# Performance work log

Hardware: AMD Instinct MI355X
Metric: run time of the kernel (lower is better)

## Reference

```python
import jax, jax.numpy as jnp
import numpy as np

B, N, C, H, W = 4, 5, 64, 100, 252  # N agents per sample (uniform record_len)


def setup_inputs() -> dict:
    key = jax.random.key(0)
    k1, k2, k3 = jax.random.split(key, 3)
    x = jax.random.normal(k1, (B * N, C, H, W), dtype=jnp.float32)
    rm = jax.random.normal(k2, (B * N, 2, H, W), dtype=jnp.float32)
    record_len = jnp.full((B,), N, dtype=jnp.int32)
    # normalized 2x3 affines (identity + small perturbation), shape (B, L, L, 2, 3)
    eye = jnp.broadcast_to(jnp.array([[1.0, 0.0, 0.0], [0.0, 1.0, 0.0]], jnp.float32), (B, N, N, 2, 3))
    pairwise_t_matrix = eye + 0.05 * jax.random.normal(k3, (B, N, N, 2, 3), dtype=jnp.float32)
    return {"x": x, "rm": rm, "record_len": record_len, "pairwise_t_matrix": pairwise_t_matrix}


def _warp_affine(feats, theta):
    # feats: (N, C, H, W), theta: (N, 2, 3). torch affine_grid + grid_sample,
    # bilinear, zeros padding, align_corners=False.
    xs = (2.0 * jnp.arange(W, dtype=jnp.float32) + 1.0) / W - 1.0
    ys = (2.0 * jnp.arange(H, dtype=jnp.float32) + 1.0) / H - 1.0
    gy, gx = jnp.meshgrid(ys, xs, indexing="ij")           # (H, W)
    base = jnp.stack([gx, gy, jnp.ones_like(gx)], axis=-1)  # (H, W, 3)
    coords = jnp.einsum("nij,hwj->nhwi", theta, base)       # (N, H, W, 2) normalized
    ix = ((coords[..., 0] + 1.0) * W - 1.0) * 0.5            # input pixel coords
    iy = ((coords[..., 1] + 1.0) * H - 1.0) * 0.5
    x0 = jnp.floor(ix); y0 = jnp.floor(iy)
    x1 = x0 + 1.0;      y1 = y0 + 1.0
    wx1 = ix - x0; wx0 = 1.0 - wx1
    wy1 = iy - y0; wy0 = 1.0 - wy1

    def gather(xi, yi):
        valid = (xi >= 0) & (xi <= W - 1) & (yi >= 0) & (yi <= H - 1)
        xc = jnp.clip(xi, 0, W - 1).astype(jnp.int32)
        yc = jnp.clip(yi, 0, H - 1).astype(jnp.int32)
        v = jax.vmap(lambda f, yy, xx: f[:, yy, xx])(feats, yc, xc)  # (N, C, H, W)
        return v * valid[:, None, :, :].astype(feats.dtype)

    out = (gather(x0, y0) * (wx0 * wy0)[:, None]
         + gather(x1, y0) * (wx1 * wy0)[:, None]
         + gather(x0, y1) * (wx0 * wy1)[:, None]
         + gather(x1, y1) * (wx1 * wy1)[:, None])
    return out  # (N, C, H, W)


def reference(x, rm, record_len, pairwise_t_matrix):
    # Where2commFusion, single-scale, MAX agg, communication disabled.
    # regroup: uniform record_len -> reshape (B, N, C, H, W)
    xr = x.reshape(B, N, C, H, W)
    theta = pairwise_t_matrix[:, 0, :, :, :]  # t_matrix[0, :N] per batch: (B, N, 2, 3)
    warped = jax.vmap(_warp_affine)(xr, theta)  # (B, N, C, H, W)
    x_fuse = jnp.max(warped, axis=1)            # (B, C, H, W)
    communication_rates = jnp.zeros((), dtype=jnp.float32)
    return (x_fuse, communication_rates)
```

## Files before the change

### kernel.cpp

```cpp
#include <hip/hip_runtime.h>
#include <math.h>

#define BB 4
#define NN 5
#define CC_DIM 64
#define HH 100
#define WW 252
#define HW (HH * WW)
#define CPT 8
#define NCHUNK (CC_DIM / CPT)

__global__ __launch_bounds__(256) void where2comm_fuse_kernel(
    const float* __restrict__ x,
    const float* __restrict__ ptm,
    float* __restrict__ out)
{
    const int idx = blockIdx.x * blockDim.x + threadIdx.x;
    const int total = BB * NCHUNK * HH * WW;
    if (idx >= total) {
        return;
    }

    int w = idx % WW;
    int t = idx / WW;
    int h = t % HH;
    t /= HH;
    int cc = t % NCHUNK;
    int b = t / NCHUNK;

    const float gx = (2.0f * (float)w + 1.0f) / (float)WW - 1.0f;
    const float gy = (2.0f * (float)h + 1.0f) / (float)HH - 1.0f;

    const float* th_b = ptm + (size_t)b * (NN * NN * 6);

    const float* pbase[NN];
    float g00[NN], g01[NN], g10[NN], g11[NN];

#pragma unroll
    for (int n = 0; n < NN; ++n) {
        const float t00 = th_b[n * 6 + 0];
        const float t01 = th_b[n * 6 + 1];
        const float t02 = th_b[n * 6 + 2];
        const float t10 = th_b[n * 6 + 3];
        const float t11 = th_b[n * 6 + 4];
        const float t12 = th_b[n * 6 + 5];

        const float cx = t00 * gx + t01 * gy + t02;
        const float cy = t10 * gx + t11 * gy + t12;

        const float ix = ((cx + 1.0f) * (float)WW - 1.0f) * 0.5f;
        const float iy = ((cy + 1.0f) * (float)HH - 1.0f) * 0.5f;

        const float x0f = floorf(ix);
        const float y0f = floorf(iy);
        const float x1f = x0f + 1.0f;
        const float y1f = y0f + 1.0f;

        const float wx1 = ix - x0f;
        const float wx0 = 1.0f - wx1;
        const float wy1 = iy - y0f;
        const float wy0 = 1.0f - wy1;

        const float mx0 = (x0f >= 0.0f && x0f <= (float)(WW - 1)) ? 1.0f : 0.0f;
        const float mx1 = (x1f >= 0.0f && x1f <= (float)(WW - 1)) ? 1.0f : 0.0f;
        const float my0 = (y0f >= 0.0f && y0f <= (float)(HH - 1)) ? 1.0f : 0.0f;
        const float my1 = (y1f >= 0.0f && y1f <= (float)(HH - 1)) ? 1.0f : 0.0f;

        const float e00 = wx0 * wy0 * mx0 * my0;
        const float e10 = wx1 * wy0 * mx1 * my0;
        const float e01 = wx0 * wy1 * mx0 * my1;
        const float e11 = wx1 * wy1 * mx1 * my1;

        const int xi0 = (int)fminf(fmaxf(x0f, 0.0f), (float)(WW - 1));
        const int xi1 = (int)fminf(fmaxf(x1f, 0.0f), (float)(WW - 1));
        const int yi0 = (int)fminf(fmaxf(y0f, 0.0f), (float)(HH - 1));
        const int yi1 = (int)fminf(fmaxf(y1f, 0.0f), (float)(HH - 1));

        const int cl = (int)fminf(fmaxf(x0f, 0.0f), (float)(WW - 2));
        const int rl = (int)fminf(fmaxf(y0f, 0.0f), (float)(HH - 2));

        const float sx0 = (float)(xi0 - cl);
        const float sx1 = (float)(xi1 - cl);
        const float sy0 = (float)(yi0 - rl);
        const float sy1 = (float)(yi1 - rl);
        const float nx0 = 1.0f - sx0, nx1 = 1.0f - sx1;
        const float ny0 = 1.0f - sy0, ny1 = 1.0f - sy1;

        g00[n] = e00 * nx0 * ny0 + e10 * nx1 * ny0 + e01 * nx0 * ny1 + e11 * nx1 * ny1;
        g01[n] = e00 * sx0 * ny0 + e10 * sx1 * ny0 + e01 * sx0 * ny1 + e11 * sx1 * ny1;
        g10[n] = e00 * nx0 * sy0 + e10 * nx1 * sy0 + e01 * nx0 * sy1 + e11 * nx1 * sy1;
        g11[n] = e00 * sx0 * sy0 + e10 * sx1 * sy0 + e01 * sx0 * sy1 + e11 * sx1 * sy1;

        pbase[n] = x + ((size_t)(b * NN + n) * CC_DIM + cc * CPT) * HW + rl * WW + cl;
    }

    float acc[CPT];
#pragma unroll
    for (int c = 0; c < CPT; ++c) acc[c] = -INFINITY;

#pragma unroll
    for (int c = 0; c < CPT; ++c) {
        float lo[NN][2], hi[NN][2];
#pragma unroll
        for (int n = 0; n < NN; ++n) {
            const float* p = pbase[n] + (size_t)c * HW;
            __builtin_memcpy(&lo[n][0], p, 8);
            __builtin_memcpy(&hi[n][0], p + WW, 8);
        }
#pragma unroll
        for (int n = 0; n < NN; ++n) {
            float v = lo[n][0] * g00[n];
            v = fmaf(lo[n][1], g01[n], v);
            v = fmaf(hi[n][0], g10[n], v);
            v = fmaf(hi[n][1], g11[n], v);
            acc[c] = fmaxf(acc[c], v);
        }
    }

#pragma unroll
    for (int c = 0; c < CPT; ++c) {
        out[(((size_t)b * CC_DIM + cc * CPT + c) * HH + h) * WW + w] = acc[c];
    }

    if (idx == 0) {
        out[(size_t)BB * CC_DIM * HW] = 0.0f;
    }
}

extern "C" void kernel_launch(void* const* d_in, const int* in_sizes, int n_in,
                              void* d_out, int out_size, void* d_ws, size_t ws_size,
                              hipStream_t stream) {
    const float* x = (const float*)d_in[0];
    const float* ptm = (const float*)d_in[3];
    float* out = (float*)d_out;

    const int total = BB * NCHUNK * HH * WW;
    const int block = 256;
    const int grid = (total + block - 1) / block;
    where2comm_fuse_kernel<<<grid, block, 0, stream>>>(x, ptm, out);
}
```

Baseline: 59.29 us.

## Stage per-channel row tiles in LDS via async global-to-LDS loads for bilinear gather

```diff
diff --git a/kernel.cpp b/kernel.cpp
--- a/kernel.cpp
+++ b/kernel.cpp
@@ -7,122 +7,151 @@
 #define HH 100
 #define WW 252
 #define HW (HH * WW)
-#define CPT 8
-#define NCHUNK (CC_DIM / CPT)
+#define TH 25
+#define NT (HH / TH)
+#define PAD 12
+#define MAXR (TH + 2 * PAD + 1)
+#define PITCH 256
 
 __global__ __launch_bounds__(256) void where2comm_fuse_kernel(
     const float* __restrict__ x,
     const float* __restrict__ ptm,
     float* __restrict__ out)
 {
-    const int idx = blockIdx.x * blockDim.x + threadIdx.x;
-    const int total = BB * NCHUNK * HH * WW;
-    if (idx >= total) {
-        return;
-    }
+    __shared__ float smem[MAXR * PITCH];
 
-    int w = idx % WW;
-    int t = idx / WW;
-    int h = t % HH;
-    t /= HH;
-    int cc = t % NCHUNK;
-    int b = t / NCHUNK;
+    const int bi = blockIdx.x;
+    const int tile = bi % NT;
+    const int c = (bi / NT) % CC_DIM;
+    const int b = bi / (NT * CC_DIM);
+
+    const int h0 = tile * TH;
+    const int lo = (h0 - PAD > 0) ? (h0 - PAD) : 0;
+    const int hi = (h0 + TH + PAD < HH - 1) ? (h0 + TH + PAD) : (HH - 1);
+    const int nrows = hi - lo + 1;
+
+    const int tid = threadIdx.x;
+    const int lane = tid & 63;
+    const int wv = tid >> 6;
+    const int w = tid;
 
     const float gx = (2.0f * (float)w + 1.0f) / (float)WW - 1.0f;
-    const float gy = (2.0f * (float)h + 1.0f) / (float)HH - 1.0f;
+    const float gy0 = (2.0f * (float)h0 + 1.0f) / (float)HH - 1.0f;
 
     const float* th_b = ptm + (size_t)b * (NN * NN * 6);
 
-    const float* pbase[NN];
-    float g00[NN], g01[NN], g10[NN], g11[NN];
+    float acc[TH];
+#pragma unroll
+    for (int r = 0; r < TH; ++r) acc[r] = -INFINITY;
+
+    for (int n = 0; n < NN; ++n) {
+        const size_t plane_f = ((size_t)(b * NN + n) * CC_DIM + c) * HW;
+
+        for (int r = wv; r < nrows; r += 4) {
+            const float* src = x + plane_f + (size_t)(lo + r) * WW + lane * 4;
+            if (lane < 63) {
+                __builtin_amdgcn_global_load_lds(
+                    (const __attribute__((address_space(1))) void*)src,
+                    (__attribute__((address_space(3))) void*)(smem + r * PITCH),
+                    16, 0, 0);
+            }
+        }
+        asm volatile("s_waitcnt vmcnt(0)" ::: "memory");
+        __syncthreads();
+
+        if (w < WW) {
+            const float t00 = th_b[n * 6 + 0];
+            const float t01 = th_b[n * 6 + 1];
+            const float t02 = th_b[n * 6 + 2];
+            const float t10 = th_b[n * 6 + 3];
+            const float t11 = th_b[n * 6 + 4];
+            const float t12 = th_b[n * 6 + 5];
+
+            const float cx0 = fmaf(t00, gx, t02);
+            const float cy0 = fmaf(t10, gx, t12);
+            const float* plane = x + plane_f;
 
 #pragma unroll
-    for (int n = 0; n < NN; ++n) {
-        const float t00 = th_b[n * 6 + 0];
-        const float t01 = th_b[n * 6 + 1];
-        const float t02 = th_b[n * 6 + 2];
-        const float t10 = th_b[n * 6 + 3];
-        const float t11 = th_b[n * 6 + 4];
-        const float t12 = th_b[n * 6 + 5];
+            for (int r = 0; r < TH; ++r) {
+                const float gyr = fmaf((float)(2 * r), 0.01f, gy0);
+                const float cx = fmaf(t01, gyr, cx0);
+                const float cy = fmaf(t11, gyr, cy0);
+                const float ix = fmaf(cx, 126.0f, 125.5f);
+                const float iy = fmaf(cy, 50.0f, 49.5f);
 
-        const float cx = t00 * gx + t01 * gy + t02;
-        const float cy = t10 * gx + t11 * gy + t12;
+                const float x0f = floorf(ix);
+                const float y0f = floorf(iy);
+                const float x1f = x0f + 1.0f;
+                const float y1f = y0f + 1.0f;
 
-        const float ix = ((cx + 1.0f) * (float)WW - 1.0f) * 0.5f;
-        const float iy = ((cy + 1.0f) * (float)HH - 1.0f) * 0.5f;
+                const float wx1 = ix - x0f;
+                const float wx0 = 1.0f - wx1;
+                const float wy1 = iy - y0f;
+                const float wy0 = 1.0f - wy1;
 
-        const float x0f = floorf(ix);
-        const float y0f = floorf(iy);
-        const float x1f = x0f + 1.0f;
-        const float y1f = y0f + 1.0f;
+                const float mx0 = (x0f >= 0.0f && x0f <= (float)(WW - 1)) ? 1.0f : 0.0f;
+                const float mx1 = (x1f >= 0.0f && x1f <= (float)(WW - 1)) ? 1.0f : 0.0f;
+                const float my0 = (y0f >= 0.0f && y0f <= (float)(HH - 1)) ? 1.0f : 0.0f;
+                const float my1 = (y1f >= 0.0f && y1f <= (float)(HH - 1)) ? 1.0f : 0.0f;
 
-        const float wx1 = ix - x0f;
-        const float wx0 = 1.0f - wx1;
-        const float wy1 = iy - y0f;
-        const float wy0 = 1.0f - wy1;
+                const float e00 = wx0 * wy0 * mx0 * my0;
+                const float e10 = wx1 * wy0 * mx1 * my0;
+                const float e01 = wx0 * wy1 * mx0 * my1;
+                const float e11 = wx1 * wy1 * mx1 * my1;
 
-        const float mx0 = (x0f >= 0.0f && x0f <= (float)(WW - 1)) ? 1.0f : 0.0f;
-        const float mx1 = (x1f >= 0.0f && x1f <= (float)(WW - 1)) ? 1.0f : 0.0f;
-        const float my0 = (y0f >= 0.0f && y0f <= (float)(HH - 1)) ? 1.0f : 0.0f;
-        const float my1 = (y1f >= 0.0f && y1f <= (float)(HH - 1)) ? 1.0f : 0.0f;
+                const int xi0 = (int)fminf(fmaxf(x0f, 0.0f), (float)(WW - 1));
+                const int xi1 = (int)fminf(fmaxf(x1f, 0.0f), (float)(WW - 1));
+                const int yi0 = (int)fminf(fmaxf(y0f, 0.0f), (float)(HH - 1));
+                const int yi1 = (int)fminf(fmaxf(y1f, 0.0f), (float)(HH - 1));
 
-        const float e00 = wx0 * wy0 * mx0 * my0;
-        const float e10 = wx1 * wy0 * mx1 * my0;
-        const float e01 = wx0 * wy1 * mx0 * my1;
-        const float e11 = wx1 * wy1 * mx1 * my1;
+                const int cl = (int)fminf(fmaxf(x0f, 0.0f), (float)(WW - 2));
+                const int rl = (int)fminf(fmaxf(y0f, 0.0f), (float)(HH - 2));
 
-        const int xi0 = (int)fminf(fmaxf(x0f, 0.0f), (float)(WW - 1));
-        const int xi1 = (int)fminf(fmaxf(x1f, 0.0f), (float)(WW - 1));
-        const int yi0 = (int)fminf(fmaxf(y0f, 0.0f), (float)(HH - 1));
-        const int yi1 = (int)fminf(fmaxf(y1f, 0.0f), (float)(HH - 1));
+                const float sx0 = (float)(xi0 - cl);
+                const float sx1 = (float)(xi1 - cl);
+                const float sy0 = (float)(yi0 - rl);
+                const float sy1 = (float)(yi1 - rl);
+                const float nx0 = 1.0f - sx0, nx1 = 1.0f - sx1;
+                const float ny0 = 1.0f - sy0, ny1 = 1.0f - sy1;
 
-        const int cl = (int)fminf(fmaxf(x0f, 0.0f), (float)(WW - 2));
-        const int rl = (int)fminf(fmaxf(y0f, 0.0f), (float)(HH - 2));
+                const float g00 = e00 * nx0 * ny0 + e10 * nx1 * ny0 + e01 * nx0 * ny1 + e11 * nx1 * ny1;
+                const float g01 = e00 * sx0 * ny0 + e10 * sx1 * ny0 + e01 * sx0 * ny1 + e11 * sx1 * ny1;
+                const float g10 = e00 * nx0 * sy0 + e10 * nx1 * sy0 + e01 * nx0 * sy1 + e11 * nx1 * sy1;
+                const float g11 = e00 * sx0 * sy0 + e10 * sx1 * sy0 + e01 * sx0 * sy1 + e11 * sx1 * sy1;
 
-        const float sx0 = (float)(xi0 - cl);
-        const float sx1 = (float)(xi1 - cl);
-        const float sy0 = (float)(yi0 - rl);
-        const float sy1 = (float)(yi1 - rl);
-        const float nx0 = 1.0f - sx0, nx1 = 1.0f - sx1;
-        const float ny0 = 1.0f - sy0, ny1 = 1.0f - sy1;
+                float l00, l01, l10, l11;
+                if (rl >= lo && rl + 1 <= hi) {
+                    const float* sp = smem + (rl - lo) * PITCH + cl;
+                    l00 = sp[0];
+                    l01 = sp[1];
+                    l10 = sp[PITCH];
+                    l11 = sp[PITCH + 1];
+                } else {
+                    const float* gp = plane + (size_t)rl * WW + cl;
+                    l00 = gp[0];
+                    l01 = gp[1];
+                    l10 = gp[WW];
+                    l11 = gp[WW + 1];
+                }
 
-        g00[n] = e00 * nx0 * ny0 + e10 * nx1 * ny0 + e01 * nx0 * ny1 + e11 * nx1 * ny1;
-        g01[n] = e00 * sx0 * ny0 + e10 * sx1 * ny0 + e01 * sx0 * ny1 + e11 * sx1 * ny1;
-        g10[n] = e00 * nx0 * sy0 + e10 * nx1 * sy0 + e01 * nx0 * sy1 + e11 * nx1 * sy1;
-        g11[n] = e00 * sx0 * sy0 + e10 * sx1 * sy0 + e01 * sx0 * sy1 + e11 * sx1 * sy1;
-
-        pbase[n] = x + ((size_t)(b * NN + n) * CC_DIM + cc * CPT) * HW + rl * WW + cl;
+                float v = l00 * g00;
+                v = fmaf(l01, g01, v);
+                v = fmaf(l10, g10, v);
+                v = fmaf(l11, g11, v);
+                acc[r] = fmaxf(acc[r], v);
+            }
+        }
+        __syncthreads();
     }
 
-    float acc[CPT];
+    if (w < WW) {
 #pragma unroll
-    for (int c = 0; c < CPT; ++c) acc[c] = -INFINITY;
-
-#pragma unroll
-    for (int c = 0; c < CPT; ++c) {
-        float lo[NN][2], hi[NN][2];
-#pragma unroll
-        for (int n = 0; n < NN; ++n) {
-            const float* p = pbase[n] + (size_t)c * HW;
-            __builtin_memcpy(&lo[n][0], p, 8);
-            __builtin_memcpy(&hi[n][0], p + WW, 8);
-        }
-#pragma unroll
-        for (int n = 0; n < NN; ++n) {
-            float v = lo[n][0] * g00[n];
-            v = fmaf(lo[n][1], g01[n], v);
-            v = fmaf(hi[n][0], g10[n], v);
-            v = fmaf(hi[n][1], g11[n], v);
-            acc[c] = fmaxf(acc[c], v);
+        for (int r = 0; r < TH; ++r) {
+            out[((size_t)(b * CC_DIM + c) * HH + h0 + r) * WW + w] = acc[r];
         }
     }
 
-#pragma unroll
-    for (int c = 0; c < CPT; ++c) {
-        out[(((size_t)b * CC_DIM + cc * CPT + c) * HH + h) * WW + w] = acc[c];
-    }
-
-    if (idx == 0) {
+    if (bi == 0 && tid == 0) {
         out[(size_t)BB * CC_DIM * HW] = 0.0f;
     }
 }
@@ -134,8 +163,6 @@
     const float* ptm = (const float*)d_in[3];
     float* out = (float*)d_out;
 
-    const int total = BB * NCHUNK * HH * WW;
-    const int block = 256;
-    const int grid = (total + block - 1) / block;
-    where2comm_fuse_kernel<<<grid, block, 0, stream>>>(x, ptm, out);
+    const int grid = BB * CC_DIM * NT;
+    where2comm_fuse_kernel<<<grid, 256, 0, stream>>>(x, ptm, out);
 }
```

Result: slower. 183.3 us (+209.1%).

## Tile rows per thread and reuse bilinear row loads across consecutive output rows

Applied to the files above, without the earlier changes.

```diff
diff --git a/kernel.cpp b/kernel.cpp
--- a/kernel.cpp
+++ b/kernel.cpp
@@ -7,122 +7,148 @@
 #define HH 100
 #define WW 252
 #define HW (HH * WW)
-#define CPT 8
-#define NCHUNK (CC_DIM / CPT)
+#define CPT 4
+#define NCC (CC_DIM / CPT)
+#define TT 5
+#define NTILE (HH / TT)
 
 __global__ __launch_bounds__(256) void where2comm_fuse_kernel(
     const float* __restrict__ x,
     const float* __restrict__ ptm,
     float* __restrict__ out)
 {
-    const int idx = blockIdx.x * blockDim.x + threadIdx.x;
-    const int total = BB * NCHUNK * HH * WW;
-    if (idx >= total) {
-        return;
-    }
+    const int bi = blockIdx.x;
+    const int tile = bi % NTILE;
+    const int cc = (bi / NTILE) % NCC;
+    const int b = bi / (NTILE * NCC);
 
-    int w = idx % WW;
-    int t = idx / WW;
-    int h = t % HH;
-    t /= HH;
-    int cc = t % NCHUNK;
-    int b = t / NCHUNK;
+    const int h0 = tile * TT;
+    const int c0 = cc * CPT;
+    const int w = threadIdx.x;
 
-    const float gx = (2.0f * (float)w + 1.0f) / (float)WW - 1.0f;
-    const float gy = (2.0f * (float)h + 1.0f) / (float)HH - 1.0f;
+    if (w < WW) {
+        const float gx = (2.0f * (float)w + 1.0f) / (float)WW - 1.0f;
 
-    const float* th_b = ptm + (size_t)b * (NN * NN * 6);
+        float gys[TT];
+#pragma unroll
+        for (int r = 0; r < TT; ++r) {
+            gys[r] = (2.0f * (float)(h0 + r) + 1.0f) / (float)HH - 1.0f;
+        }
 
-    const float* pbase[NN];
-    float g00[NN], g01[NN], g10[NN], g11[NN];
+        const float* th_b = ptm + (size_t)b * (NN * NN * 6);
+
+        float acc[CPT][TT];
+#pragma unroll
+        for (int c = 0; c < CPT; ++c) {
+#pragma unroll
+            for (int r = 0; r < TT; ++r) acc[c][r] = -INFINITY;
+        }
 
 #pragma unroll
-    for (int n = 0; n < NN; ++n) {
-        const float t00 = th_b[n * 6 + 0];
-        const float t01 = th_b[n * 6 + 1];
-        const float t02 = th_b[n * 6 + 2];
-        const float t10 = th_b[n * 6 + 3];
-        const float t11 = th_b[n * 6 + 4];
-        const float t12 = th_b[n * 6 + 5];
+        for (int n = 0; n < NN; ++n) {
+            const float t00 = th_b[n * 6 + 0];
+            const float t01 = th_b[n * 6 + 1];
+            const float t02 = th_b[n * 6 + 2];
+            const float t10 = th_b[n * 6 + 3];
+            const float t11 = th_b[n * 6 + 4];
+            const float t12 = th_b[n * 6 + 5];
 
-        const float cx = t00 * gx + t01 * gy + t02;
-        const float cy = t10 * gx + t11 * gy + t12;
+            const float* plane = x + ((size_t)(b * NN + n) * CC_DIM + c0) * HW;
 
-        const float ix = ((cx + 1.0f) * (float)WW - 1.0f) * 0.5f;
-        const float iy = ((cy + 1.0f) * (float)HH - 1.0f) * 0.5f;
-
-        const float x0f = floorf(ix);
-        const float y0f = floorf(iy);
-        const float x1f = x0f + 1.0f;
-        const float y1f = y0f + 1.0f;
-
-        const float wx1 = ix - x0f;
-        const float wx0 = 1.0f - wx1;
-        const float wy1 = iy - y0f;
-        const float wy0 = 1.0f - wy1;
-
-        const float mx0 = (x0f >= 0.0f && x0f <= (float)(WW - 1)) ? 1.0f : 0.0f;
-        const float mx1 = (x1f >= 0.0f && x1f <= (float)(WW - 1)) ? 1.0f : 0.0f;
-        const float my0 = (y0f >= 0.0f && y0f <= (float)(HH - 1)) ? 1.0f : 0.0f;
-        const float my1 = (y1f >= 0.0f && y1f <= (float)(HH - 1)) ? 1.0f : 0.0f;
-
-        const float e00 = wx0 * wy0 * mx0 * my0;
-        const float e10 = wx1 * wy0 * mx1 * my0;
-        const float e01 = wx0 * wy1 * mx0 * my1;
-        const float e11 = wx1 * wy1 * mx1 * my1;
-
-        const int xi0 = (int)fminf(fmaxf(x0f, 0.0f), (float)(WW - 1));
-        const int xi1 = (int)fminf(fmaxf(x1f, 0.0f), (float)(WW - 1));
-        const int yi0 = (int)fminf(fmaxf(y0f, 0.0f), (float)(HH - 1));
-        const int yi1 = (int)fminf(fmaxf(y1f, 0.0f), (float)(HH - 1));
-
-        const int cl = (int)fminf(fmaxf(x0f, 0.0f), (float)(WW - 2));
-        const int rl = (int)fminf(fmaxf(y0f, 0.0f), (float)(HH - 2));
-
-        const float sx0 = (float)(xi0 - cl);
-        const float sx1 = (float)(xi1 - cl);
-        const float sy0 = (float)(yi0 - rl);
-        const float sy1 = (float)(yi1 - rl);
-        const float nx0 = 1.0f - sx0, nx1 = 1.0f - sx1;
-        const float ny0 = 1.0f - sy0, ny1 = 1.0f - sy1;
-
-        g00[n] = e00 * nx0 * ny0 + e10 * nx1 * ny0 + e01 * nx0 * ny1 + e11 * nx1 * ny1;
-        g01[n] = e00 * sx0 * ny0 + e10 * sx1 * ny0 + e01 * sx0 * ny1 + e11 * sx1 * ny1;
-        g10[n] = e00 * nx0 * sy0 + e10 * nx1 * sy0 + e01 * nx0 * sy1 + e11 * nx1 * sy1;
-        g11[n] = e00 * sx0 * sy0 + e10 * sx1 * sy0 + e01 * sx0 * sy1 + e11 * sx1 * sy1;
-
-        pbase[n] = x + ((size_t)(b * NN + n) * CC_DIM + cc * CPT) * HW + rl * WW + cl;
-    }
-
-    float acc[CPT];
-#pragma unroll
-    for (int c = 0; c < CPT; ++c) acc[c] = -INFINITY;
+            float lo[CPT][2], hi[CPT][2];
+            int carry_rl = -1000, carry_cl = -1000;
 
 #pragma unroll
-    for (int c = 0; c < CPT; ++c) {
-        float lo[NN][2], hi[NN][2];
+            for (int r = 0; r < TT; ++r) {
+                const float gyr = gys[r];
+                const float cx = t00 * gx + t01 * gyr + t02;
+                const float cy = t10 * gx + t11 * gyr + t12;
+                const float ix = ((cx + 1.0f) * (float)WW - 1.0f) * 0.5f;
+                const float iy = ((cy + 1.0f) * (float)HH - 1.0f) * 0.5f;
+
+                const float x0f = floorf(ix);
+                const float y0f = floorf(iy);
+                const float x1f = x0f + 1.0f;
+                const float y1f = y0f + 1.0f;
+
+                const float wx1 = ix - x0f;
+                const float wx0 = 1.0f - wx1;
+                const float wy1 = iy - y0f;
+                const float wy0 = 1.0f - wy1;
+
+                const float mx0 = (x0f >= 0.0f && x0f <= (float)(WW - 1)) ? 1.0f : 0.0f;
+                const float mx1 = (x1f >= 0.0f && x1f <= (float)(WW - 1)) ? 1.0f : 0.0f;
+                const float my0 = (y0f >= 0.0f && y0f <= (float)(HH - 1)) ? 1.0f : 0.0f;
+                const float my1 = (y1f >= 0.0f && y1f <= (float)(HH - 1)) ? 1.0f : 0.0f;
+
+                const float e00 = wx0 * wy0 * mx0 * my0;
+                const float e10 = wx1 * wy0 * mx1 * my0;
+                const float e01 = wx0 * wy1 * mx0 * my1;
+                const float e11 = wx1 * wy1 * mx1 * my1;
+
+                const int xi0 = (int)fminf(fmaxf(x0f, 0.0f), (float)(WW - 1));
+                const int xi1 = (int)fminf(fmaxf(x1f, 0.0f), (float)(WW - 1));
+                const int yi0 = (int)fminf(fmaxf(y0f, 0.0f), (float)(HH - 1));
+                const int yi1 = (int)fminf(fmaxf(y1f, 0.0f), (float)(HH - 1));
+
+                const int cl = (int)fminf(fmaxf(x0f, 0.0f), (float)(WW - 2));
+                const int rl = (int)fminf(fmaxf(y0f, 0.0f), (float)(HH - 2));
+
+                const float sx0 = (float)(xi0 - cl);
+                const float sx1 = (float)(xi1 - cl);
+                const float sy0 = (float)(yi0 - rl);
+                const float sy1 = (float)(yi1 - rl);
+                const float nx0 = 1.0f - sx0, nx1 = 1.0f - sx1;
+                const float ny0 = 1.0f - sy0, ny1 = 1.0f - sy1;
+
+                const float g00 = e00 * nx0 * ny0 + e10 * nx1 * ny0 + e01 * nx0 * ny1 + e11 * nx1 * ny1;
+                const float g01 = e00 * sx0 * ny0 + e10 * sx1 * ny0 + e01 * sx0 * ny1 + e11 * sx1 * ny1;
+                const float g10 = e00 * nx0 * sy0 + e10 * nx1 * sy0 + e01 * nx0 * sy1 + e11 * nx1 * sy1;
+                const float g11 = e00 * sx0 * sy0 + e10 * sx1 * sy0 + e01 * sx0 * sy1 + e11 * sx1 * sy1;
+
+                const int off = rl * WW + cl;
+                const bool same  = (rl == carry_rl) && (cl == carry_cl);
+                const bool shift = (rl == carry_rl + 1) && (cl == carry_cl);
+                if (!same) {
+                    if (shift) {
 #pragma unroll
-        for (int n = 0; n < NN; ++n) {
-            const float* p = pbase[n] + (size_t)c * HW;
-            __builtin_memcpy(&lo[n][0], p, 8);
-            __builtin_memcpy(&hi[n][0], p + WW, 8);
+                        for (int c = 0; c < CPT; ++c) {
+                            lo[c][0] = hi[c][0];
+                            lo[c][1] = hi[c][1];
+                            __builtin_memcpy(&hi[c][0], plane + (size_t)c * HW + off + WW, 8);
+                        }
+                    } else {
+#pragma unroll
+                        for (int c = 0; c < CPT; ++c) {
+                            __builtin_memcpy(&lo[c][0], plane + (size_t)c * HW + off, 8);
+                            __builtin_memcpy(&hi[c][0], plane + (size_t)c * HW + off + WW, 8);
+                        }
+                    }
+                }
+                carry_rl = rl;
+                carry_cl = cl;
+
+#pragma unroll
+                for (int c = 0; c < CPT; ++c) {
+                    float v = lo[c][0] * g00;
+                    v = fmaf(lo[c][1], g01, v);
+                    v = fmaf(hi[c][0], g10, v);
+                    v = fmaf(hi[c][1], g11, v);
+                    acc[c][r] = fmaxf(acc[c][r], v);
+                }
+            }
         }
+
 #pragma unroll
-        for (int n = 0; n < NN; ++n) {
-            float v = lo[n][0] * g00[n];
-            v = fmaf(lo[n][1], g01[n], v);
-            v = fmaf(hi[n][0], g10[n], v);
-            v = fmaf(hi[n][1], g11[n], v);
-            acc[c] = fmaxf(acc[c], v);
+        for (int c = 0; c < CPT; ++c) {
+#pragma unroll
+            for (int r = 0; r < TT; ++r) {
+                out[((size_t)(b * CC_DIM + c0 + c) * HH + h0 + r) * WW + w] = acc[c][r];
+            }
         }
     }
 
-#pragma unroll
-    for (int c = 0; c < CPT; ++c) {
-        out[(((size_t)b * CC_DIM + cc * CPT + c) * HH + h) * WW + w] = acc[c];
-    }
-
-    if (idx == 0) {
+    if (bi == 0 && threadIdx.x == 0) {
         out[(size_t)BB * CC_DIM * HW] = 0.0f;
     }
 }
@@ -134,8 +160,6 @@
     const float* ptm = (const float*)d_in[3];
     float* out = (float*)d_out;
 
-    const int total = BB * NCHUNK * HH * WW;
-    const int block = 256;
-    const int grid = (total + block - 1) / block;
-    where2comm_fuse_kernel<<<grid, block, 0, stream>>>(x, ptm, out);
+    const int grid = BB * NCC * NTILE;
+    where2comm_fuse_kernel<<<grid, 256, 0, stream>>>(x, ptm, out);
 }
```

Measured after the change: 148.8 us. +151.0%, slower.
